# Performance work log

Hardware: AMD Instinct MI355X
Metric: run time of the kernel (lower is better)

## Reference

```python
import jax, jax.numpy as jnp
import numpy as np
from jax.scipy.special import logsumexp

B, F, V, C, K, KP = 8192, 32, 64, 32, 8, 7  # batch, features, values/feature, classes, gate options, padded pair candidates
TEMP = 1.0
EPS = 1e-06


def _structure():
    # candidate 0 = self table; candidates 1..7 = pair tables conditioned on preceding features
    mask = np.zeros((F - 1, K), dtype=bool)
    mask[:, 0] = True
    cond = np.zeros((F - 1, KP), dtype=np.int32)
    for i in range(F - 1):
        fi = i + 1
        for j in range(min(fi, KP)):
            mask[i, j + 1] = True
            cond[i, j] = fi - 1 - j
    return jnp.asarray(cond), jnp.asarray(mask)


def setup_inputs() -> dict:
    key = jax.random.key(0)
    ks = jax.random.split(key, 6)
    cond_index, valid_mask = _structure()
    return {
        "x": jax.random.randint(ks[0], (B, F), 0, V, dtype=jnp.int32),
        "training": True,
        "class_logits": jax.random.normal(ks[1], (C,), jnp.float32) * 0.1,
        "table0": jax.random.normal(ks[2], (V, C), jnp.float32) * 0.1,
        "self_tables": jax.random.normal(ks[3], (F - 1, V, C), jnp.float32) * 0.1,
        "pair_tables": jax.random.normal(ks[4], (F - 1, KP, V, V, C), jnp.float32) * 0.1,
        "structure_logits": jax.random.normal(ks[5], (F - 1, K), jnp.float32) * 0.1,
        "u_noise": jax.random.uniform(jax.random.fold_in(key, 7), (F - 1, K), jnp.float32),
        "cond_index": cond_index,
        "valid_mask": valid_mask,
    }


def reference(x, training, class_logits, table0, self_tables, pair_tables,
              structure_logits, u_noise, cond_index, valid_mask):
    # class prior term
    cl = class_logits - logsumexp(class_logits)  # [C]
    t0 = table0 - logsumexp(table0, axis=0, keepdims=True)  # [V,C]
    out = cl[None, :] + t0[x[:, 0]]  # [B,C]

    # Gumbel-softmax gate over candidate parent sets (training path)
    g = -jnp.log(-jnp.log(u_noise + EPS) + EPS)
    gate_logits = jnp.where(valid_mask, (structure_logits + g) / TEMP, -jnp.inf)
    w = jax.nn.softmax(gate_logits, axis=-1)  # [F-1,K]; padded entries get weight 0

    f_idx = jnp.arange(F - 1)
    xs = x[:, 1:]  # [B,F-1] feature values

    # self (class-only) candidate tables, normalized over the feature-value axis
    st = self_tables - logsumexp(self_tables, axis=1, keepdims=True)  # [F-1,V,C]
    self_g = st[f_idx[None, :], xs]  # [B,F-1,C]
    out = out + jnp.einsum('bfc,f->bc', self_g, w[:, 0])

    # pair candidate tables, normalized over the feature-value axis (axis 2)
    pt = pair_tables - logsumexp(pair_tables, axis=2, keepdims=True)  # [F-1,KP,V,V,C]
    xc = x[:, cond_index]  # [B,F-1,KP] conditioning feature values
    k_idx = jnp.arange(KP)
    pair_g = pt[f_idx[None, :, None], k_idx[None, None, :], xs[:, :, None], xc]  # [B,F-1,KP,C]
    out = out + jnp.einsum('bfkc,fk->bc', pair_g, w[:, 1:])
    return out
```

## Files before the change

### kernel.cpp

```cpp
#include <hip/hip_runtime.h>
#include <math.h>

#define B_  8192
#define F_  32
#define V_  64
#define C_  32
#define KP_ 7
#define EPS_ 1e-6f

typedef float f4 __attribute__((ext_vector_type(4)));

#define WS_OFF  256
#define WS_G    512
#define WS_LSE  66048
#define LSE_BANK4 111104
#define WS_PART 1843712

#define NBLK_LSE 868
#define NBLK_PAIR 2048

__device__ const int d_split[9] = {0, 25, 50, 74, 99, 123, 148, 172, 196};

__global__ __launch_bounds__(256)
void fused_kernel(const int* __restrict__ x, const float* __restrict__ pt,
                  const float* __restrict__ cl, const float* __restrict__ t0,
                  const float* __restrict__ st, const float* __restrict__ sl,
                  const float* __restrict__ un, float* __restrict__ ws) {
    if (blockIdx.x < NBLK_LSE) {
        int fk = blockIdx.x >> 2;
        int qa = blockIdx.x & 3;
        int t  = threadIdx.x;
        const f4* __restrict__ p =
            (const f4*)(pt + (size_t)fk * (V_ * V_ * C_)
                           + (size_t)qa * 16 * (V_ * C_));
        const f4* p0 = p + t;
        const f4* p1 = p + 256 + t;
        f4 s0 = (f4)(0.f);
        f4 s1 = (f4)(0.f);
        #pragma unroll 4
        for (int a = 0; a < 16; a++) {
            f4 l0 = __builtin_nontemporal_load(p0 + a * 512);
            f4 l1 = __builtin_nontemporal_load(p1 + a * 512);
            s0.x += __expf(l0.x); s0.y += __expf(l0.y);
            s0.z += __expf(l0.z); s0.w += __expf(l0.w);
            s1.x += __expf(l1.x); s1.y += __expf(l1.y);
            s1.z += __expf(l1.z); s1.w += __expf(l1.w);
        }
        f4* lseP = (f4*)(ws + WS_LSE) + (size_t)qa * LSE_BANK4;
        __builtin_nontemporal_store(s0, lseP + fk * 512 + t);
        __builtin_nontemporal_store(s1, lseP + fk * 512 + 256 + t);
    } else if (blockIdx.x == NBLK_LSE) {
        __shared__ float gl[31][8];
        __shared__ float wsm[31][8];
        __shared__ float lsf[31][32];
        int tid = threadIdx.x;
        if (tid < 248) {
            int f = tid >> 3, k = tid & 7;
            int kmax = min(f + 1, KP_);
            bool valid = (k <= kmax);
            float u = un[tid];
            float g = -__logf(-__logf(u + EPS_) + EPS_);
            gl[f][k] = valid ? (sl[tid] + g) : -INFINITY;
        } else {
            ws[tid] = 0.f;
        }
        __syncthreads();
        if (tid < 248) {
            int f = tid >> 3, k = tid & 7;
            float m = -INFINITY;
            #pragma unroll
            for (int j = 0; j < 8; j++) m = fmaxf(m, gl[f][j]);
            float s = 0.f;
            #pragma unroll
            for (int j = 0; j < 8; j++) s += __expf(gl[f][j] - m);
            float wv = __expf(gl[f][k] - m) / s;
            wsm[f][k] = wv;
            ws[tid] = wv;
        }
        for (int i = tid; i < 992; i += 256) {
            int f = i >> 5, c = i & 31;
            float s = 0.f;
            #pragma unroll 8
            for (int v = 0; v < V_; v++) s += __expf(st[(f * V_ + v) * C_ + c]);
            lsf[f][c] = __logf(s);
        }
        __syncthreads();
        if (tid < 32) {
            int c = tid;
            float scl = 0.f;
            #pragma unroll
            for (int j = 0; j < C_; j++) scl += __expf(cl[j]);
            float lse_cl = __logf(scl);
            float s0 = 0.f;
            #pragma unroll 8
            for (int v = 0; v < V_; v++) s0 += __expf(t0[v * C_ + c]);
            float lse_t0 = __logf(s0);
            float acc = cl[c] - lse_cl - lse_t0;
            for (int f = 0; f < 31; f++) acc -= wsm[f][0] * lsf[f][c];
            ws[WS_OFF + c] = acc;
        }
    } else {
        __shared__ int    xsh[4 * 33];
        __shared__ float  wsh[256];
        __shared__ int    etab[200];
        __shared__ float4 part[7][32];
        __shared__ float  gl[31][8];
        int tid = threadIdx.x;
        int pb  = blockIdx.x - (NBLK_LSE + 1);
        if (tid < 128) xsh[(tid >> 5) * 33 + (tid & 31)] = x[pb * 128 + tid];
        if (tid < 248) {
            int f = tid >> 3, k = tid & 7;
            int kmax = min(f + 1, KP_);
            bool valid = (k <= kmax);
            float u = un[tid];
            float g = -__logf(-__logf(u + EPS_) + EPS_);
            gl[f][k] = valid ? (sl[tid] + g) : -INFINITY;
        }
        if (tid < 200) {
            int q = tid / 25, i = tid % 25;
            int g = d_split[q] + i;
            int packed;
            if (g < d_split[q + 1]) {
                int f = 0, base = 0;
                for (;;) { int cnt = min(f + 1, KP_); if (g < base + cnt) break; base += cnt; f++; }
                int k = g - base;
                packed = ((f * 8 + k + 1) << 20) | ((f * KP_ + k) << 12) | ((f + 1) << 6) | (f - k);
            } else {
                packed = (248 << 20);
            }
            etab[tid] = packed;
        }
        __syncthreads();
        if (tid < 248) {
            int f = tid >> 3;
            float m = -INFINITY;
            #pragma unroll
            for (int j = 0; j < 8; j++) m = fmaxf(m, gl[f][j]);
            float s = 0.f;
            #pragma unroll
            for (int j = 0; j < 8; j++) s += __expf(gl[f][j] - m);
            wsh[tid] = __expf(gl[f][tid & 7] - m) / s;
        } else {
            wsh[tid] = 0.f;
        }
        __syncthreads();

        int q  = tid >> 5;
        int r  = (tid >> 3) & 3;
        int c4 = tid & 7;
        const int* xrow = &xsh[r * 33];
        const float* __restrict__ ptb = pt + c4 * 4;
        float4 acc = make_float4(0.f, 0.f, 0.f, 0.f);

        int beg = q * 25;
        #pragma unroll
        for (int ch = 0; ch < 5; ch++) {
            float4 pv[5];
            float  wt[5];
            #pragma unroll
            for (int i = 0; i < 5; i++) {
                int pk = etab[beg + ch * 5 + i];
                int ci = pk & 63, fi = (pk >> 6) & 63;
                int fk = (pk >> 12) & 255, widx = (pk >> 20) & 255;
                int xv = xrow[fi], xc = xrow[ci];
                pv[i] = *(const float4*)(ptb + ((size_t)(fk * V_ + xv) * V_ + xc) * C_);
                wt[i] = wsh[widx];
            }
            #pragma unroll
            for (int i = 0; i < 5; i++) {
                acc.x += wt[i] * pv[i].x; acc.y += wt[i] * pv[i].y;
                acc.z += wt[i] * pv[i].z; acc.w += wt[i] * pv[i].w;
            }
        }

        if (q > 0) part[q - 1][r * 8 + c4] = acc;
        __syncthreads();
        if (q == 0) {
            #pragma unroll
            for (int p = 0; p < 7; p++) {
                float4 pv2 = part[p][r * 8 + c4];
                acc.x += pv2.x; acc.y += pv2.y; acc.z += pv2.z; acc.w += pv2.w;
            }
            ((float4*)(ws + WS_PART))[(pb * 4 + r) * 8 + c4] = acc;
        }
    }
}

__global__ __launch_bounds__(256)
void foldg_kernel(const float* __restrict__ t0, const float* __restrict__ st,
                  float* __restrict__ ws) {
    int idx = blockIdx.x * 256 + threadIdx.x;
    int c4 = idx & 7, v = (idx >> 3) & 63, j = idx >> 9;
    int nk = min(KP_, 31 - j);
    const float4* lse4 = (const float4*)(ws + WS_LSE);
    float4 g;
    if (j == 0) {
        g = ((const float4*)t0)[v * 8 + c4];
    } else {
        float w0 = ws[(j - 1) * 8];
        float4 sv = ((const float4*)st)[((j - 1) * V_ + v) * 8 + c4];
        g.x = w0 * sv.x; g.y = w0 * sv.y; g.z = w0 * sv.z; g.w = w0 * sv.w;
    }
    for (int k = 0; k < nk; k++) {
        int f = j + k;
        float wv = ws[f * 8 + k + 1];
        int iq = ((f * KP_ + k) * V_ + v) * 8 + c4;
        float4 sa = lse4[iq];
        float4 sb = lse4[1 * LSE_BANK4 + iq];
        float4 sc = lse4[2 * LSE_BANK4 + iq];
        float4 sd = lse4[3 * LSE_BANK4 + iq];
        g.x -= wv * __logf(sa.x + sb.x + sc.x + sd.x);
        g.y -= wv * __logf(sa.y + sb.y + sc.y + sd.y);
        g.z -= wv * __logf(sa.z + sb.z + sc.z + sd.z);
        g.w -= wv * __logf(sa.w + sb.w + sc.w + sd.w);
    }
    ((float4*)(ws + WS_G))[idx] = g;
}

__global__ __launch_bounds__(256)
void maing_kernel(const int* __restrict__ x, const float* __restrict__ ws,
                  float* __restrict__ out) {
    __shared__ int    xsh[32][33];
    __shared__ float4 offv[8];
    int tid = threadIdx.x;
    int rbase = blockIdx.x * 32;
    for (int i = tid; i < 1024; i += 256) {
        int rr = i >> 5, jj = i & 31;
        xsh[rr][jj] = x[(rbase + rr) * 32 + jj];
    }
    if (tid < 8) offv[tid] = ((const float4*)(ws + WS_OFF))[tid];
    __syncthreads();
    int r = tid >> 3, c4 = tid & 7;
    const float4* __restrict__ G4 = (const float4*)(ws + WS_G);
    float4 acc = ((const float4*)(ws + WS_PART))[(rbase + r) * 8 + c4];
    float4 ov = offv[c4];
    acc.x += ov.x; acc.y += ov.y; acc.z += ov.z; acc.w += ov.w;
    #pragma unroll 8
    for (int j = 0; j < 32; j++) {
        float4 gv = G4[(j * V_ + xsh[r][j]) * 8 + c4];
        acc.x += gv.x; acc.y += gv.y; acc.z += gv.z; acc.w += gv.w;
    }
    ((float4*)out)[(rbase + r) * 8 + c4] = acc;
}

extern "C" void kernel_launch(void* const* d_in, const int* in_sizes, int n_in,
                              void* d_out, int out_size, void* d_ws, size_t ws_size,
                              hipStream_t stream) {
    const int*   x   = (const int*)  d_in[0];
    const float* cl  = (const float*)d_in[2];
    const float* t0  = (const float*)d_in[3];
    const float* st  = (const float*)d_in[4];
    const float* pt  = (const float*)d_in[5];
    const float* sl  = (const float*)d_in[6];
    const float* un  = (const float*)d_in[7];
    float* ws  = (float*)d_ws;
    float* out = (float*)d_out;

    fused_kernel<<<NBLK_LSE + 1 + NBLK_PAIR, 256, 0, stream>>>(x, pt, cl, t0, st, sl, un, ws);
    foldg_kernel<<<64, 256, 0, stream>>>(t0, st, ws);
    maing_kernel<<<256, 256, 0, stream>>>(x, ws, out);
}
```

Baseline: 223.2 us.

## Split pair gathers by entry group across blocks, reduce partials in main kernel

Each pair block now handles 32 samples and one of eight entry groups, where previously it handled 4 samples across all eight groups. This removes the in-block shared-memory reduction and its barrier. The eight per-group partials are written to the workspace and summed later in maing_kernel. The cost is eight times more partial-sum traffic through global memory and extra loads in the main kernel. The trade is fewer in-block syncs and better reuse of the x tile in exchange for that traffic.

After: 221.3 us (median of 2 runs). Within noise of the previous version (-0.9%).

```diff
diff --git a/kernel.cpp b/kernel.cpp
--- a/kernel.cpp
+++ b/kernel.cpp
@@ -100,30 +100,33 @@
             ws[WS_OFF + c] = acc;
         }
     } else {
-        __shared__ int    xsh[4 * 33];
-        __shared__ float  wsh[256];
-        __shared__ int    etab[200];
-        __shared__ float4 part[7][32];
-        __shared__ float  gl[31][8];
+        __shared__ int   xsh[32][33];
+        __shared__ float wsh[256];
+        __shared__ int   etab[200];
+        __shared__ float gl[31][8];
         int tid = threadIdx.x;
-        int pb  = blockIdx.x - (NBLK_LSE + 1);
-        if (tid < 128) xsh[(tid >> 5) * 33 + (tid & 31)] = x[pb * 128 + tid];
+        int pb    = blockIdx.x - (NBLK_LSE + 1);
+        int g     = pb & 7;
+        int chunk = pb >> 3;
+        int s0    = chunk * 32;
+        for (int i = tid; i < 1024; i += 256)
+            xsh[i >> 5][i & 31] = x[s0 * 32 + i];
         if (tid < 248) {
             int f = tid >> 3, k = tid & 7;
             int kmax = min(f + 1, KP_);
             bool valid = (k <= kmax);
             float u = un[tid];
-            float g = -__logf(-__logf(u + EPS_) + EPS_);
-            gl[f][k] = valid ? (sl[tid] + g) : -INFINITY;
+            float gg = -__logf(-__logf(u + EPS_) + EPS_);
+            gl[f][k] = valid ? (sl[tid] + gg) : -INFINITY;
         }
         if (tid < 200) {
             int q = tid / 25, i = tid % 25;
-            int g = d_split[q] + i;
+            int e = d_split[q] + i;
             int packed;
-            if (g < d_split[q + 1]) {
+            if (e < d_split[q + 1]) {
                 int f = 0, base = 0;
-                for (;;) { int cnt = min(f + 1, KP_); if (g < base + cnt) break; base += cnt; f++; }
-                int k = g - base;
+                for (;;) { int cnt = min(f + 1, KP_); if (e < base + cnt) break; base += cnt; f++; }
+                int k = e - base;
                 packed = ((f * 8 + k + 1) << 20) | ((f * KP_ + k) << 12) | ((f + 1) << 6) | (f - k);
             } else {
                 packed = (248 << 20);
@@ -145,14 +148,13 @@
         }
         __syncthreads();
 
-        int q  = tid >> 5;
-        int r  = (tid >> 3) & 3;
+        int s  = tid >> 3;
         int c4 = tid & 7;
-        const int* xrow = &xsh[r * 33];
+        const int* xrow = xsh[s];
         const float* __restrict__ ptb = pt + c4 * 4;
         float4 acc = make_float4(0.f, 0.f, 0.f, 0.f);
 
-        int beg = q * 25;
+        int beg = g * 25;
         #pragma unroll
         for (int ch = 0; ch < 5; ch++) {
             float4 pv[5];
@@ -172,17 +174,7 @@
                 acc.z += wt[i] * pv[i].z; acc.w += wt[i] * pv[i].w;
             }
         }
-
-        if (q > 0) part[q - 1][r * 8 + c4] = acc;
-        __syncthreads();
-        if (q == 0) {
-            #pragma unroll
-            for (int p = 0; p < 7; p++) {
-                float4 pv2 = part[p][r * 8 + c4];
-                acc.x += pv2.x; acc.y += pv2.y; acc.z += pv2.z; acc.w += pv2.w;
-            }
-            ((float4*)(ws + WS_PART))[(pb * 4 + r) * 8 + c4] = acc;
-        }
+        ((float4*)(ws + WS_PART))[(size_t)(s0 + s) * 64 + g * 8 + c4] = acc;
     }
 }
 
@@ -232,9 +224,14 @@
     __syncthreads();
     int r = tid >> 3, c4 = tid & 7;
     const float4* __restrict__ G4 = (const float4*)(ws + WS_G);
-    float4 acc = ((const float4*)(ws + WS_PART))[(rbase + r) * 8 + c4];
-    float4 ov = offv[c4];
-    acc.x += ov.x; acc.y += ov.y; acc.z += ov.z; acc.w += ov.w;
+    float4 acc = offv[c4];
+    const float4* __restrict__ pp =
+        (const float4*)(ws + WS_PART) + (size_t)(rbase + r) * 64 + c4;
+    #pragma unroll
+    for (int g = 0; g < 8; g++) {
+        float4 t = pp[g * 8];
+        acc.x += t.x; acc.y += t.y; acc.z += t.z; acc.w += t.w;
+    }
     #pragma unroll 8
     for (int j = 0; j < 32; j++) {
         float4 gv = G4[(j * V_ + xsh[r][j]) * 8 + c4];
```
